# Performance work log

Measured on AMD Instinct MI355X. Metric: run time of the kernel, lower is better.

Reference implementation:

```python
import jax, jax.numpy as jnp
import numpy as np


def setup_inputs() -> dict:
    key = jax.random.key(0)
    k1, k2, k3 = jax.random.split(key, 3)
    M, P, K = 4096, 64, 128
    color_seqs = jax.random.normal(k1, (M, P, K), dtype=jnp.float32)
    mew = jax.random.normal(k2, (M, K), dtype=jnp.float32)
    sigma = jax.random.normal(k3, (M, K, K), dtype=jnp.float32)
    return {"color_seqs": color_seqs, "mew": mew, "sigma": sigma}


def reference(color_seqs, mew, sigma):
    # shifted: (m, p, k)
    shifted = color_seqs - mew[:, None, :]
    # scores[m,p] = - (c-mu) Sigma (c-mu)^T  (negated batched quadratic form)
    scores = -jnp.einsum('mpk,mkl,mpl->mp', shifted, sigma, shifted)
    # softmax over the context (p) dimension, matching nn.Softmax(dim=1)
    return jax.nn.softmax(scores, axis=1)
```

## Files before the change

### kernel.cpp

```cpp
#include <hip/hip_runtime.h>

#define SROW 132

typedef _Float16 half8 __attribute__((ext_vector_type(8)));
typedef float f32x4 __attribute__((ext_vector_type(4)));


__global__ __launch_bounds__(256, 2)
void quadform_softmax(const float* __restrict__ color,
                      const float* __restrict__ mew,
                      const float* __restrict__ sigma,
                      float* __restrict__ out) {
  __shared__ __align__(16) float s_all[4 * 16 * SROW];
  __shared__ __align__(16) _Float16 Bp[2][2][8][64][8];
  __shared__ float scores_lds[64];

  const int tid  = threadIdx.x;
  const int wv   = tid >> 6;
  const int lane = tid & 63;
  const int m    = blockIdx.x;

  float* sw = &s_all[wv * (16 * SROW)];
  const float* sg = sigma + (size_t)m * 16384;

  const int c0 = tid & 63;
  const int h  = tid >> 6;

  float pre[16];
#pragma unroll
  for (int i = 0; i < 8; ++i) pre[i]     = sg[(size_t)(8 * h + i) * 128 + c0];
#pragma unroll
  for (int i = 0; i < 8; ++i) pre[8 + i] = sg[(size_t)(8 * h + i) * 128 + c0 + 64];

  {
    const int hh = lane >> 5;
    const int q  = lane & 31;
    const float4* c4 = reinterpret_cast<const float4*>(color + (size_t)m * 8192)
                       + (size_t)(16 * wv) * 32;
    const float4 mw = reinterpret_cast<const float4*>(mew + (size_t)m * 128)[q];
#pragma unroll
    for (int r = 0; r < 8; ++r) {
      const int row = hh + 2 * r;
      float4 v = c4[row * 32 + q];
      v.x -= mw.x; v.y -= mw.y; v.z -= mw.z; v.w -= mw.w;
      *reinterpret_cast<float4*>(&sw[row * SROW + 4 * q]) = v;
    }
  }

  auto stage_write = [&](int buf) {
    half8 hi0, lo0, hi1, lo1;
#pragma unroll
    for (int i = 0; i < 8; ++i) {
      float x = pre[i];
      _Float16 xh = (_Float16)x;
      hi0[i] = xh;
      lo0[i] = (_Float16)(x - (float)xh);
      float y = pre[8 + i];
      _Float16 yh = (_Float16)y;
      hi1[i] = yh;
      lo1[i] = (_Float16)(y - (float)yh);
    }
    const int t0 = c0 >> 4, r0 = c0 & 15, slot = h * 16 + r0;
    *reinterpret_cast<half8*>(&Bp[buf][0][t0    ][slot][0]) = hi0;
    *reinterpret_cast<half8*>(&Bp[buf][1][t0    ][slot][0]) = lo0;
    *reinterpret_cast<half8*>(&Bp[buf][0][t0 + 4][slot][0]) = hi1;
    *reinterpret_cast<half8*>(&Bp[buf][1][t0 + 4][slot][0]) = lo1;
  };

  stage_write(0);
  __syncthreads();

  f32x4 acc[8];
#pragma unroll
  for (int t = 0; t < 8; ++t) acc[t] = (f32x4){0.f, 0.f, 0.f, 0.f};

  const int hl = lane >> 4;
  const int rl = lane & 15;

#pragma unroll 1
  for (int ch = 0; ch < 4; ++ch) {
    const int kc = ch * 32;
    if (ch < 3) {
      const float* gn = sg + (size_t)(kc + 32) * 128;
#pragma unroll
      for (int i = 0; i < 8; ++i) pre[i]     = gn[(size_t)(8 * h + i) * 128 + c0];
#pragma unroll
      for (int i = 0; i < 8; ++i) pre[8 + i] = gn[(size_t)(8 * h + i) * 128 + c0 + 64];
    }

    half8 ah, al;
    {
      const float* sa = &sw[rl * SROW + kc + 8 * hl];
      float4 a0 = *reinterpret_cast<const float4*>(sa);
      float4 a1 = *reinterpret_cast<const float4*>(sa + 4);
      float av[8] = {a0.x, a0.y, a0.z, a0.w, a1.x, a1.y, a1.z, a1.w};
#pragma unroll
      for (int j = 0; j < 8; ++j) {
        _Float16 xh = (_Float16)av[j];
        ah[j] = xh;
        al[j] = (_Float16)(av[j] - (float)xh);
      }
    }

    const int buf = ch & 1;
#pragma unroll
    for (int t = 0; t < 8; ++t) {
      half8 bh = *reinterpret_cast<const half8*>(&Bp[buf][0][t][lane][0]);
      half8 bl = *reinterpret_cast<const half8*>(&Bp[buf][1][t][lane][0]);
      acc[t] = __builtin_amdgcn_mfma_f32_16x16x32_f16(ah, bh, acc[t], 0, 0, 0);
      acc[t] = __builtin_amdgcn_mfma_f32_16x16x32_f16(ah, bl, acc[t], 0, 0, 0);
      acc[t] = __builtin_amdgcn_mfma_f32_16x16x32_f16(al, bh, acc[t], 0, 0, 0);
    }

    if (ch < 3) stage_write(buf ^ 1);
    __syncthreads();
  }

  float part[4] = {0.f, 0.f, 0.f, 0.f};
#pragma unroll
  for (int t = 0; t < 8; ++t) {
#pragma unroll
    for (int r = 0; r < 4; ++r) {
      float sv = sw[(4 * hl + r) * SROW + 16 * t + rl];
      part[r] = fmaf(acc[t][r], sv, part[r]);
    }
  }
#pragma unroll
  for (int r = 0; r < 4; ++r) {
    part[r] += __shfl_xor(part[r], 1, 64);
    part[r] += __shfl_xor(part[r], 2, 64);
    part[r] += __shfl_xor(part[r], 4, 64);
    part[r] += __shfl_xor(part[r], 8, 64);
  }
  if (rl == 0) {
#pragma unroll
    for (int r = 0; r < 4; ++r)
      scores_lds[wv * 16 + 4 * hl + r] = -part[r];
  }
  __syncthreads();

  if (tid < 64) {
    float sc = scores_lds[tid];
    float mx = sc;
#pragma unroll
    for (int off = 1; off < 64; off <<= 1) mx = fmaxf(mx, __shfl_xor(mx, off, 64));
    float e = __expf(sc - mx);
    float s = e;
#pragma unroll
    for (int off = 1; off < 64; off <<= 1) s += __shfl_xor(s, off, 64);
    out[(size_t)m * 64 + tid] = e / s;
  }
}

extern "C" void kernel_launch(void* const* d_in, const int* in_sizes, int n_in,
                              void* d_out, int out_size, void* d_ws, size_t ws_size,
                              hipStream_t stream) {
  const float* color = (const float*)d_in[0];
  const float* mew   = (const float*)d_in[1];
  const float* sigma = (const float*)d_in[2];
  float* out = (float*)d_out;
  const int M = in_sizes[1] / 128;
  quadform_softmax<<<M, 256, 0, stream>>>(color, mew, sigma, out);
}
```

Baseline: 429.6 us.

## Single-buffer sigma staging, prebuild A fragments, raise occupancy to three blocks

Halves the LDS staging buffer for the fp16-split sigma tile from double to single buffering, adding an extra barrier per chunk. All four A-operand hi/lo fragments are built once up front and the chunk loop is fully unrolled with macros. Launch bounds now target three blocks per CU, so more blocks can hide global-load latency. The cost is tighter register pressure and an extra sync per chunk.

```diff
diff --git a/kernel.cpp b/kernel.cpp
--- a/kernel.cpp
+++ b/kernel.cpp
@@ -6,13 +6,13 @@
 typedef float f32x4 __attribute__((ext_vector_type(4)));
 
 
-__global__ __launch_bounds__(256, 2)
+__global__ __launch_bounds__(256, 3)
 void quadform_softmax(const float* __restrict__ color,
                       const float* __restrict__ mew,
                       const float* __restrict__ sigma,
                       float* __restrict__ out) {
   __shared__ __align__(16) float s_all[4 * 16 * SROW];
-  __shared__ __align__(16) _Float16 Bp[2][2][8][64][8];
+  __shared__ __align__(16) _Float16 Bp[2][8][64][8];
   __shared__ float scores_lds[64];
 
   const int tid  = threadIdx.x;
@@ -21,16 +21,44 @@
   const int m    = blockIdx.x;
 
   float* sw = &s_all[wv * (16 * SROW)];
-  const float* sg = sigma + (size_t)m * 16384;
+  const float* sg  = sigma + (size_t)m * 16384;
+  const float* sgh = sg + wv * (8 * 128);
 
-  const int c0 = tid & 63;
-  const int h  = tid >> 6;
+  float p0,p1,p2,p3,p4,p5,p6,p7,p8,p9,p10,p11,p12,p13,p14,p15;
 
-  float pre[16];
-#pragma unroll
-  for (int i = 0; i < 8; ++i) pre[i]     = sg[(size_t)(8 * h + i) * 128 + c0];
-#pragma unroll
-  for (int i = 0; i < 8; ++i) pre[8 + i] = sg[(size_t)(8 * h + i) * 128 + c0 + 64];
+#define SIG_LOAD(CH) do {                                               \
+    const float* gp = sgh + (CH) * (32 * 128);                          \
+    p0  = gp[0*128 + lane];       p1  = gp[1*128 + lane];               \
+    p2  = gp[2*128 + lane];       p3  = gp[3*128 + lane];               \
+    p4  = gp[4*128 + lane];       p5  = gp[5*128 + lane];               \
+    p6  = gp[6*128 + lane];       p7  = gp[7*128 + lane];               \
+    p8  = gp[0*128 + 64 + lane];  p9  = gp[1*128 + 64 + lane];          \
+    p10 = gp[2*128 + 64 + lane];  p11 = gp[3*128 + 64 + lane];          \
+    p12 = gp[4*128 + 64 + lane];  p13 = gp[5*128 + 64 + lane];          \
+    p14 = gp[6*128 + 64 + lane];  p15 = gp[7*128 + 64 + lane];          \
+  } while (0)
+
+#define CV(H, L, I, X) do { _Float16 t_ = (_Float16)(X);                \
+    H[I] = t_; L[I] = (_Float16)((X) - (float)t_); } while (0)
+
+#define SIG_WRITE() do {                                                \
+    half8 hi0, lo0, hi1, lo1;                                           \
+    CV(hi0, lo0, 0, p0);  CV(hi0, lo0, 1, p1);                          \
+    CV(hi0, lo0, 2, p2);  CV(hi0, lo0, 3, p3);                          \
+    CV(hi0, lo0, 4, p4);  CV(hi0, lo0, 5, p5);                          \
+    CV(hi0, lo0, 6, p6);  CV(hi0, lo0, 7, p7);                          \
+    CV(hi1, lo1, 0, p8);  CV(hi1, lo1, 1, p9);                          \
+    CV(hi1, lo1, 2, p10); CV(hi1, lo1, 3, p11);                         \
+    CV(hi1, lo1, 4, p12); CV(hi1, lo1, 5, p13);                         \
+    CV(hi1, lo1, 6, p14); CV(hi1, lo1, 7, p15);                         \
+    const int t0_ = lane >> 4, slot_ = wv * 16 + (lane & 15);           \
+    *reinterpret_cast<half8*>(&Bp[0][t0_    ][slot_][0]) = hi0;         \
+    *reinterpret_cast<half8*>(&Bp[1][t0_    ][slot_][0]) = lo0;         \
+    *reinterpret_cast<half8*>(&Bp[0][t0_ + 4][slot_][0]) = hi1;         \
+    *reinterpret_cast<half8*>(&Bp[1][t0_ + 4][slot_][0]) = lo1;         \
+  } while (0)
+
+  SIG_LOAD(0);
 
   {
     const int hh = lane >> 5;
@@ -47,74 +75,64 @@
     }
   }
 
-  auto stage_write = [&](int buf) {
-    half8 hi0, lo0, hi1, lo1;
-#pragma unroll
-    for (int i = 0; i < 8; ++i) {
-      float x = pre[i];
-      _Float16 xh = (_Float16)x;
-      hi0[i] = xh;
-      lo0[i] = (_Float16)(x - (float)xh);
-      float y = pre[8 + i];
-      _Float16 yh = (_Float16)y;
-      hi1[i] = yh;
-      lo1[i] = (_Float16)(y - (float)yh);
-    }
-    const int t0 = c0 >> 4, r0 = c0 & 15, slot = h * 16 + r0;
-    *reinterpret_cast<half8*>(&Bp[buf][0][t0    ][slot][0]) = hi0;
-    *reinterpret_cast<half8*>(&Bp[buf][1][t0    ][slot][0]) = lo0;
-    *reinterpret_cast<half8*>(&Bp[buf][0][t0 + 4][slot][0]) = hi1;
-    *reinterpret_cast<half8*>(&Bp[buf][1][t0 + 4][slot][0]) = lo1;
-  };
+  const int hl = lane >> 4;
+  const int rl = lane & 15;
+  half8 aH0, aL0, aH1, aL1, aH2, aL2, aH3, aL3;
 
-  stage_write(0);
+#define A_BUILD(Q, AH, AL) do {                                         \
+    const float* sa_ = &sw[rl * SROW + (Q) * 32 + 8 * hl];              \
+    float4 x0_ = *reinterpret_cast<const float4*>(sa_);                 \
+    float4 x1_ = *reinterpret_cast<const float4*>(sa_ + 4);             \
+    CV(AH, AL, 0, x0_.x); CV(AH, AL, 1, x0_.y);                         \
+    CV(AH, AL, 2, x0_.z); CV(AH, AL, 3, x0_.w);                         \
+    CV(AH, AL, 4, x1_.x); CV(AH, AL, 5, x1_.y);                         \
+    CV(AH, AL, 6, x1_.z); CV(AH, AL, 7, x1_.w);                         \
+  } while (0)
+
+  A_BUILD(0, aH0, aL0);
+  A_BUILD(1, aH1, aL1);
+  A_BUILD(2, aH2, aL2);
+  A_BUILD(3, aH3, aL3);
+
+  SIG_WRITE();
   __syncthreads();
 
   f32x4 acc[8];
 #pragma unroll
   for (int t = 0; t < 8; ++t) acc[t] = (f32x4){0.f, 0.f, 0.f, 0.f};
 
-  const int hl = lane >> 4;
-  const int rl = lane & 15;
+#define MT(T, AH, AL) do {                                                    \
+    half8 bh_ = *reinterpret_cast<const half8*>(&Bp[0][T][lane][0]);          \
+    half8 bl_ = *reinterpret_cast<const half8*>(&Bp[1][T][lane][0]);          \
+    acc[T] = __builtin_amdgcn_mfma_f32_16x16x32_f16(AH, bh_, acc[T], 0,0,0);  \
+    acc[T] = __builtin_amdgcn_mfma_f32_16x16x32_f16(AH, bl_, acc[T], 0,0,0);  \
+    acc[T] = __builtin_amdgcn_mfma_f32_16x16x32_f16(AL, bh_, acc[T], 0,0,0);  \
+  } while (0)
 
-#pragma unroll 1
-  for (int ch = 0; ch < 4; ++ch) {
-    const int kc = ch * 32;
-    if (ch < 3) {
-      const float* gn = sg + (size_t)(kc + 32) * 128;
-#pragma unroll
-      for (int i = 0; i < 8; ++i) pre[i]     = gn[(size_t)(8 * h + i) * 128 + c0];
-#pragma unroll
-      for (int i = 0; i < 8; ++i) pre[8 + i] = gn[(size_t)(8 * h + i) * 128 + c0 + 64];
-    }
+#define MFMA_CHUNK(AH, AL) do {                                         \
+    MT(0, AH, AL); MT(1, AH, AL); MT(2, AH, AL); MT(3, AH, AL);         \
+    MT(4, AH, AL); MT(5, AH, AL); MT(6, AH, AL); MT(7, AH, AL);         \
+  } while (0)
 
-    half8 ah, al;
-    {
-      const float* sa = &sw[rl * SROW + kc + 8 * hl];
-      float4 a0 = *reinterpret_cast<const float4*>(sa);
-      float4 a1 = *reinterpret_cast<const float4*>(sa + 4);
-      float av[8] = {a0.x, a0.y, a0.z, a0.w, a1.x, a1.y, a1.z, a1.w};
-#pragma unroll
-      for (int j = 0; j < 8; ++j) {
-        _Float16 xh = (_Float16)av[j];
-        ah[j] = xh;
-        al[j] = (_Float16)(av[j] - (float)xh);
-      }
-    }
+  SIG_LOAD(1);
+  MFMA_CHUNK(aH0, aL0);
+  __syncthreads();
+  SIG_WRITE();
+  __syncthreads();
 
-    const int buf = ch & 1;
-#pragma unroll
-    for (int t = 0; t < 8; ++t) {
-      half8 bh = *reinterpret_cast<const half8*>(&Bp[buf][0][t][lane][0]);
-      half8 bl = *reinterpret_cast<const half8*>(&Bp[buf][1][t][lane][0]);
-      acc[t] = __builtin_amdgcn_mfma_f32_16x16x32_f16(ah, bh, acc[t], 0, 0, 0);
-      acc[t] = __builtin_amdgcn_mfma_f32_16x16x32_f16(ah, bl, acc[t], 0, 0, 0);
-      acc[t] = __builtin_amdgcn_mfma_f32_16x16x32_f16(al, bh, acc[t], 0, 0, 0);
-    }
+  SIG_LOAD(2);
+  MFMA_CHUNK(aH1, aL1);
+  __syncthreads();
+  SIG_WRITE();
+  __syncthreads();
 
-    if (ch < 3) stage_write(buf ^ 1);
-    __syncthreads();
-  }
+  SIG_LOAD(3);
+  MFMA_CHUNK(aH2, aL2);
+  __syncthreads();
+  SIG_WRITE();
+  __syncthreads();
+
+  MFMA_CHUNK(aH3, aL3);
 
   float part[4] = {0.f, 0.f, 0.f, 0.f};
 #pragma unroll
```

Result: no change. 431.9 us (+0.5%).
